# Kernel tuning notes

Measured on AMD Instinct MI355X. Metric: run time of the kernel, lower is better.

Reference implementation:

```python
import jax, jax.numpy as jnp
import numpy as np

N_NODES = 100000
N_EDGES = 1600000
D_IN = 128
D_HID = 128


def spmm(edge_row, edge_col, edge_val, x):
    # sparse [N,N] @ dense [N,D]: out[r] += val * x[c]
    gathered = edge_val[:, None] * x[edge_col]  # [E, D]
    return jax.ops.segment_sum(gathered, edge_row, num_segments=N_NODES)


def setup_inputs() -> dict:
    key = jax.random.key(0)
    ks = jax.random.split(key, 8)
    x = jax.random.normal(ks[0], (N_NODES, D_IN), dtype=jnp.float32)
    edge_row = jax.random.randint(ks[1], (N_EDGES,), 0, N_NODES, dtype=jnp.int32)
    edge_col = jax.random.randint(ks[2], (N_EDGES,), 0, N_NODES, dtype=jnp.int32)
    edge_val = jax.random.uniform(ks[3], (N_EDGES,), dtype=jnp.float32)
    s1 = 1.0 / np.sqrt(D_IN)
    s2 = 1.0 / np.sqrt(D_HID)
    W1 = jax.random.normal(ks[4], (D_IN, D_HID), dtype=jnp.float32) * s1
    b1 = jnp.zeros((D_HID,), dtype=jnp.float32)
    W2 = jax.random.normal(ks[5], (D_HID, D_HID), dtype=jnp.float32) * s2
    b2 = jnp.zeros((D_HID,), dtype=jnp.float32)
    Wout = jax.random.normal(ks[6], (D_HID, 1), dtype=jnp.float32) * s2
    bout = jnp.zeros((1,), dtype=jnp.float32)
    return {"x": x, "edge_row": edge_row, "edge_col": edge_col,
            "edge_val": edge_val, "W1": W1, "b1": b1, "W2": W2, "b2": b2,
            "Wout": Wout, "bout": bout}


def reference(x, edge_row, edge_col, edge_val, W1, b1, W2, b2, Wout, bout):
    # Layer 1: SpMM -> Linear -> ReLU (dropout = identity in eval)
    h = spmm(edge_row, edge_col, edge_val, x)
    h = jax.nn.relu(h @ W1 + b1)
    # Layer 2
    h = spmm(edge_row, edge_col, edge_val, h)
    h = jax.nn.relu(h @ W2 + b2)
    h = spmm(edge_row, edge_col, edge_val, h)
    out = h @ Wout + bout
    return jax.nn.softplus(out)
```

## Files before the change

### kernel.cpp

```cpp
#include <hip/hip_runtime.h>
#include <math.h>


typedef unsigned int u32;
typedef unsigned short u16;

__device__ inline float bf2f(u32 lo16){ return __uint_as_float(lo16 << 16); }
__device__ inline u32 f2bf(float f){
  u32 t = __float_as_uint(f);
  return (t + 0x7FFFu + ((t >> 16) & 1u)) >> 16;
}

__global__ void k_hist(const int* __restrict__ row, int* __restrict__ cnt, int E){
  int e = blockIdx.x*256 + threadIdx.x;
  if(e < E) atomicAdd(&cnt[__builtin_nontemporal_load(&row[e])], 1);
}

__global__ void k_scan1(const int* __restrict__ cnt, int* __restrict__ scanned,
                        int* __restrict__ sums, int n){
  __shared__ int tmp[1024];
  int i = blockIdx.x*1024 + threadIdx.x;
  int v = (i<n)? cnt[i] : 0;
  tmp[threadIdx.x] = v;
  __syncthreads();
  for(int off=1; off<1024; off<<=1){
    int t = (threadIdx.x>=off)? tmp[threadIdx.x-off] : 0;
    __syncthreads();
    tmp[threadIdx.x] += t;
    __syncthreads();
  }
  if(i<n) scanned[i] = tmp[threadIdx.x] - v;
  if(threadIdx.x==1023) sums[blockIdx.x] = tmp[1023];
}

__global__ void k_scan2(int* sums, int ntiles){
  if(threadIdx.x==0 && blockIdx.x==0){
    int acc=0;
    for(int i=0;i<ntiles;i++){ int v=sums[i]; sums[i]=acc; acc+=v; }
  }
}

__global__ void k_scan3(const int* __restrict__ scanned, const int* __restrict__ sums,
                        int* __restrict__ row_ptr, int* __restrict__ offs, int n, int E){
  int i = blockIdx.x*256 + threadIdx.x;
  if(i<n){ int ex = scanned[i] + sums[i>>10]; row_ptr[i]=ex; offs[i]=ex; }
  else if(i==n){ row_ptr[n]=E; }
}

__global__ __launch_bounds__(256) void k_scatter(const int* __restrict__ row,
                          const int* __restrict__ col,
                          const float* __restrict__ val, int* __restrict__ offs,
                          int2* __restrict__ pairs, int E, int N){
  const int r   = blockIdx.x & 7;
  const int sb  = blockIdx.x >> 3;
  const int nsb = gridDim.x >> 3;
  const int rpr = (N + 7) >> 3;
  const int lo  = r * rpr;
  const int hi  = min(lo + rpr, N);
  const int stride = nsb * 256;
  for(int e = sb*256 + threadIdx.x; e < E; e += stride){
    int rw = __builtin_nontemporal_load(&row[e]);
    if(rw >= lo && rw < hi){
      int   c = __builtin_nontemporal_load(&col[e]);
      float v = __builtin_nontemporal_load(&val[e]);
      int p = atomicAdd(&offs[rw], 1);
      pairs[p] = make_int2(c, __float_as_int(v));
    }
  }
}

template<bool A_BF16>
__global__ __launch_bounds__(256) void k_gemm(const void* __restrict__ Xv,
                                              const float* __restrict__ W,
                                              u16* __restrict__ Y, int n){
  __shared__ float xs_t[32][128];
  __shared__ float ws[32][128];
  const int t    = threadIdx.x;
  const int row0 = blockIdx.x * 128;
  const int cg   = t & 15;
  const int rg   = t >> 4;

  float acc[8][8];
  #pragma unroll
  for(int i=0;i<8;i++)
    #pragma unroll
    for(int j=0;j<8;j++) acc[i][j]=0.f;

  for(int kt=0; kt<128; kt+=32){
    {
      int r = t>>1, q = t&1;
      int gr = row0 + r;
      int kb = q*16;
      if(A_BF16){
        const u16* Xb = (const u16*)Xv;
        uint4 a = make_uint4(0,0,0,0), b = a;
        if(gr < n){
          const uint4* src = (const uint4*)(Xb + (size_t)gr*128 + kt + q*16);
          a = src[0]; b = src[1];
        }
        xs_t[kb+ 0][r]=bf2f(a.x&0xffff); xs_t[kb+ 1][r]=bf2f(a.x>>16);
        xs_t[kb+ 2][r]=bf2f(a.y&0xffff); xs_t[kb+ 3][r]=bf2f(a.y>>16);
        xs_t[kb+ 4][r]=bf2f(a.z&0xffff); xs_t[kb+ 5][r]=bf2f(a.z>>16);
        xs_t[kb+ 6][r]=bf2f(a.w&0xffff); xs_t[kb+ 7][r]=bf2f(a.w>>16);
        xs_t[kb+ 8][r]=bf2f(b.x&0xffff); xs_t[kb+ 9][r]=bf2f(b.x>>16);
        xs_t[kb+10][r]=bf2f(b.y&0xffff); xs_t[kb+11][r]=bf2f(b.y>>16);
        xs_t[kb+12][r]=bf2f(b.z&0xffff); xs_t[kb+13][r]=bf2f(b.z>>16);
        xs_t[kb+14][r]=bf2f(b.w&0xffff); xs_t[kb+15][r]=bf2f(b.w>>16);
      }else{
        const float* Xf = (const float*)Xv;
        float4 a = make_float4(0,0,0,0), b = a, c = a, d = a;
        if(gr < n){
          const float4* src = (const float4*)(Xf + (size_t)gr*128 + kt + q*16);
          a = src[0]; b = src[1]; c = src[2]; d = src[3];
        }
        xs_t[kb+ 0][r]=a.x; xs_t[kb+ 1][r]=a.y; xs_t[kb+ 2][r]=a.z; xs_t[kb+ 3][r]=a.w;
        xs_t[kb+ 4][r]=b.x; xs_t[kb+ 5][r]=b.y; xs_t[kb+ 6][r]=b.z; xs_t[kb+ 7][r]=b.w;
        xs_t[kb+ 8][r]=c.x; xs_t[kb+ 9][r]=c.y; xs_t[kb+10][r]=c.z; xs_t[kb+11][r]=c.w;
        xs_t[kb+12][r]=d.x; xs_t[kb+13][r]=d.y; xs_t[kb+14][r]=d.z; xs_t[kb+15][r]=d.w;
      }
    }
    #pragma unroll
    for(int rep=0; rep<4; rep++){
      int f  = t + rep*256;
      int kr = f >> 5;
      int cq = f & 31;
      float4 w = *(const float4*)(W + (size_t)(kt+kr)*128 + cq*4);
      *(float4*)&ws[kr][cq*4] = w;
    }
    __syncthreads();

    #pragma unroll
    for(int kk=0; kk<32; kk++){
      float4 wv0 = *(const float4*)&ws[kk][cg*8];
      float4 wv1 = *(const float4*)&ws[kk][cg*8+4];
      #pragma unroll
      for(int i=0;i<8;i++){
        float xv = xs_t[kk][rg*8+i];
        acc[i][0] = fmaf(xv, wv0.x, acc[i][0]);
        acc[i][1] = fmaf(xv, wv0.y, acc[i][1]);
        acc[i][2] = fmaf(xv, wv0.z, acc[i][2]);
        acc[i][3] = fmaf(xv, wv0.w, acc[i][3]);
        acc[i][4] = fmaf(xv, wv1.x, acc[i][4]);
        acc[i][5] = fmaf(xv, wv1.y, acc[i][5]);
        acc[i][6] = fmaf(xv, wv1.z, acc[i][6]);
        acc[i][7] = fmaf(xv, wv1.w, acc[i][7]);
      }
    }
    __syncthreads();
  }

  #pragma unroll
  for(int i=0;i<8;i++){
    int gr = row0 + rg*8 + i;
    if(gr < n){
      u32 w0 = f2bf(acc[i][0]) | (f2bf(acc[i][1])<<16);
      u32 w1 = f2bf(acc[i][2]) | (f2bf(acc[i][3])<<16);
      u32 w2 = f2bf(acc[i][4]) | (f2bf(acc[i][5])<<16);
      u32 w3 = f2bf(acc[i][6]) | (f2bf(acc[i][7])<<16);
      *(uint4*)(Y + (size_t)gr*128 + cg*8) = make_uint4(w0,w1,w2,w3);
    }
  }
}

__global__ __launch_bounds__(256) void k_spmm_relu(const int* __restrict__ row_ptr,
                                                   const int2* __restrict__ pairs,
                                                   const u16* __restrict__ y,
                                                   const float* __restrict__ bias,
                                                   u16* __restrict__ h, int n){
  int wid  = (int)((blockIdx.x*(size_t)blockDim.x + threadIdx.x) >> 6);
  int lane = threadIdx.x & 63;
  if(wid >= n) return;
  int s = row_ptr[wid], e = row_ptr[wid+1];
  float ax0=0.f, ay0=0.f, ax1=0.f, ay1=0.f, ax2=0.f, ay2=0.f, ax3=0.f, ay3=0.f;
  int i = s;
  for(; i+4 <= e; i += 4){
    int2 p0 = pairs[i], p1 = pairs[i+1], p2 = pairs[i+2], p3 = pairs[i+3];
    u32 w0 = ((const u32*)(y + (size_t)p0.x*128))[lane];
    u32 w1 = ((const u32*)(y + (size_t)p1.x*128))[lane];
    u32 w2 = ((const u32*)(y + (size_t)p2.x*128))[lane];
    u32 w3 = ((const u32*)(y + (size_t)p3.x*128))[lane];
    float v0 = __int_as_float(p0.y), v1 = __int_as_float(p1.y);
    float v2 = __int_as_float(p2.y), v3 = __int_as_float(p3.y);
    ax0 = fmaf(v0, bf2f(w0&0xffff), ax0); ay0 = fmaf(v0, bf2f(w0>>16), ay0);
    ax1 = fmaf(v1, bf2f(w1&0xffff), ax1); ay1 = fmaf(v1, bf2f(w1>>16), ay1);
    ax2 = fmaf(v2, bf2f(w2&0xffff), ax2); ay2 = fmaf(v2, bf2f(w2>>16), ay2);
    ax3 = fmaf(v3, bf2f(w3&0xffff), ax3); ay3 = fmaf(v3, bf2f(w3>>16), ay3);
  }
  for(; i < e; i++){
    int2 p = pairs[i];
    float v = __int_as_float(p.y);
    u32 w = ((const u32*)(y + (size_t)p.x*128))[lane];
    ax0 = fmaf(v, bf2f(w&0xffff), ax0); ay0 = fmaf(v, bf2f(w>>16), ay0);
  }
  float accx = (ax0+ax1)+(ax2+ax3);
  float accy = (ay0+ay1)+(ay2+ay3);
  float2 b = ((const float2*)bias)[lane];
  accx = fmaxf(accx + b.x, 0.f);
  accy = fmaxf(accy + b.y, 0.f);
  ((u32*)(h + (size_t)wid*128))[lane] = f2bf(accx) | (f2bf(accy)<<16);
}

__global__ __launch_bounds__(256) void k_spmm_head(const int* __restrict__ row_ptr,
                                                   const int2* __restrict__ pairs,
                                                   const u16* __restrict__ y,
                                                   const float* __restrict__ bias,
                                                   const float* __restrict__ Wout,
                                                   float* __restrict__ z, int n){
  int wid  = (int)((blockIdx.x*(size_t)blockDim.x + threadIdx.x) >> 6);
  int lane = threadIdx.x & 63;
  if(wid >= n) return;
  int s = row_ptr[wid], e = row_ptr[wid+1];
  float ax0=0.f, ay0=0.f, ax1=0.f, ay1=0.f, ax2=0.f, ay2=0.f, ax3=0.f, ay3=0.f;
  int i = s;
  for(; i+4 <= e; i += 4){
    int2 p0 = pairs[i], p1 = pairs[i+1], p2 = pairs[i+2], p3 = pairs[i+3];
    u32 w0 = ((const u32*)(y + (size_t)p0.x*128))[lane];
    u32 w1 = ((const u32*)(y + (size_t)p1.x*128))[lane];
    u32 w2 = ((const u32*)(y + (size_t)p2.x*128))[lane];
    u32 w3 = ((const u32*)(y + (size_t)p3.x*128))[lane];
    float v0 = __int_as_float(p0.y), v1 = __int_as_float(p1.y);
    float v2 = __int_as_float(p2.y), v3 = __int_as_float(p3.y);
    ax0 = fmaf(v0, bf2f(w0&0xffff), ax0); ay0 = fmaf(v0, bf2f(w0>>16), ay0);
    ax1 = fmaf(v1, bf2f(w1&0xffff), ax1); ay1 = fmaf(v1, bf2f(w1>>16), ay1);
    ax2 = fmaf(v2, bf2f(w2&0xffff), ax2); ay2 = fmaf(v2, bf2f(w2>>16), ay2);
    ax3 = fmaf(v3, bf2f(w3&0xffff), ax3); ay3 = fmaf(v3, bf2f(w3>>16), ay3);
  }
  for(; i < e; i++){
    int2 p = pairs[i];
    float v = __int_as_float(p.y);
    u32 w = ((const u32*)(y + (size_t)p.x*128))[lane];
    ax0 = fmaf(v, bf2f(w&0xffff), ax0); ay0 = fmaf(v, bf2f(w>>16), ay0);
  }
  float accx = (ax0+ax1)+(ax2+ax3);
  float accy = (ay0+ay1)+(ay2+ay3);
  float2 b  = ((const float2*)bias)[lane];
  float2 wv = ((const float2*)Wout)[lane];
  float hx = fmaxf(accx + b.x, 0.f);
  float hy = fmaxf(accy + b.y, 0.f);
  float p = hx*wv.x + hy*wv.y;
  #pragma unroll
  for(int off=32; off; off>>=1) p += __shfl_down(p, off);
  if(lane==0) z[wid] = p;
}

__global__ void k_spmm1_softplus(const int* __restrict__ row_ptr,
                                 const int2* __restrict__ pairs,
                                 const float* __restrict__ z,
                                 const float* __restrict__ bout,
                                 float* __restrict__ out, int n){
  int r = blockIdx.x*256 + threadIdx.x;
  if(r >= n) return;
  int s = row_ptr[r], e = row_ptr[r+1];
  float a0=0.f, a1=0.f, a2=0.f, a3=0.f;
  int i = s;
  for(; i+4 <= e; i += 4){
    int2 p0 = pairs[i],   p1 = pairs[i+1], p2 = pairs[i+2], p3 = pairs[i+3];
    a0 = fmaf(__int_as_float(p0.y), z[p0.x], a0);
    a1 = fmaf(__int_as_float(p1.y), z[p1.x], a1);
    a2 = fmaf(__int_as_float(p2.y), z[p2.x], a2);
    a3 = fmaf(__int_as_float(p3.y), z[p3.x], a3);
  }
  for(; i < e; i++){
    int2 p = pairs[i];
    a0 = fmaf(__int_as_float(p.y), z[p.x], a0);
  }
  float x = (a0+a1)+(a2+a3) + bout[0];
  out[r] = fmaxf(x, 0.f) + log1pf(expf(-fabsf(x)));
}

extern "C" void kernel_launch(void* const* d_in, const int* in_sizes, int n_in,
                              void* d_out, int out_size, void* d_ws, size_t ws_size,
                              hipStream_t stream){
  const float* x    = (const float*)d_in[0];
  const int*   erow = (const int*)d_in[1];
  const int*   ecol = (const int*)d_in[2];
  const float* eval = (const float*)d_in[3];
  const float* W1   = (const float*)d_in[4];
  const float* b1   = (const float*)d_in[5];
  const float* W2   = (const float*)d_in[6];
  const float* b2   = (const float*)d_in[7];
  const float* Wout = (const float*)d_in[8];
  const float* bout = (const float*)d_in[9];
  float* out = (float*)d_out;

  const int N = in_sizes[0] / 128;
  const int E = in_sizes[1];

  char* p = (char*)d_ws;
  auto alloc = [&](size_t bytes)->char*{
    char* r = p; p += (bytes + 255) & ~(size_t)255; return r;
  };
  int*   cnt     = (int*)  alloc((size_t)N*4);
  int*   row_ptr = (int*)  alloc((size_t)(N+1)*4);
  int*   offs    = (int*)  alloc((size_t)N*4);
  int*   scanned = (int*)  alloc((size_t)N*4);
  int*   sums    = (int*)  alloc(4096);
  int2*  pairs   = (int2*) alloc((size_t)E*8);
  u16*   ybuf    = (u16*)  alloc((size_t)N*128*2);
  u16*   hbuf    = (u16*)  alloc((size_t)N*128*2);
  float* z       = (float*)alloc((size_t)N*4);

  hipMemsetAsync(cnt, 0, (size_t)N*4, stream);
  k_hist<<<(E+255)/256, 256, 0, stream>>>(erow, cnt, E);
  int ntiles = (N+1023)/1024;
  k_scan1<<<ntiles, 1024, 0, stream>>>(cnt, scanned, sums, N);
  k_scan2<<<1, 64, 0, stream>>>(sums, ntiles);
  k_scan3<<<(N+1+255)/256, 256, 0, stream>>>(scanned, sums, row_ptr, offs, N, E);
  k_scatter<<<1024, 256, 0, stream>>>(erow, ecol, eval, offs, pairs, E, N);

  k_gemm<false><<<(N+127)/128, 256, 0, stream>>>(x, W1, ybuf, N);
  k_spmm_relu<<<(N+3)/4, 256, 0, stream>>>(row_ptr, pairs, ybuf, b1, hbuf, N);
  k_gemm<true><<<(N+127)/128, 256, 0, stream>>>(hbuf, W2, ybuf, N);
  k_spmm_head<<<(N+3)/4, 256, 0, stream>>>(row_ptr, pairs, ybuf, b2, Wout, z, N);
  k_spmm1_softplus<<<(N+255)/256, 256, 0, stream>>>(row_ptr, pairs, z, bout, out, N);
}
```

Measured before the change: 526.1 us.

## Replace FP32 FMA GEMM with bf16 MFMA GEMM using pre-transposed bf16 weights

The dense 128x128 GEMM now runs on bf16 MFMA instructions instead of scalar FP32 FMAs. The whole A tile and the weight matrix are staged in LDS with an XOR swizzle to avoid bank conflicts, and the weights are pre-converted and transposed by a small new kernel. Rounding the FP32 input x and the weights to bf16 adds precision loss, and the scalar per-element output stores are less coalesced than before. Nontemporal loads on row are also dropped in the hist and scatter kernels.

```diff
diff --git a/kernel.cpp b/kernel.cpp
--- a/kernel.cpp
+++ b/kernel.cpp
@@ -4,6 +4,8 @@
 
 typedef unsigned int u32;
 typedef unsigned short u16;
+typedef __attribute__((ext_vector_type(8))) short bf16x8;
+typedef __attribute__((ext_vector_type(4))) float f32x4;
 
 __device__ inline float bf2f(u32 lo16){ return __uint_as_float(lo16 << 16); }
 __device__ inline u32 f2bf(float f){
@@ -13,7 +15,7 @@
 
 __global__ void k_hist(const int* __restrict__ row, int* __restrict__ cnt, int E){
   int e = blockIdx.x*256 + threadIdx.x;
-  if(e < E) atomicAdd(&cnt[__builtin_nontemporal_load(&row[e])], 1);
+  if(e < E) atomicAdd(&cnt[row[e]], 1);
 }
 
 __global__ void k_scan1(const int* __restrict__ cnt, int* __restrict__ scanned,
@@ -59,7 +61,7 @@
   const int hi  = min(lo + rpr, N);
   const int stride = nsb * 256;
   for(int e = sb*256 + threadIdx.x; e < E; e += stride){
-    int rw = __builtin_nontemporal_load(&row[e]);
+    int rw = row[e];
     if(rw >= lo && rw < hi){
       int   c = __builtin_nontemporal_load(&col[e]);
       float v = __builtin_nontemporal_load(&val[e]);
@@ -69,95 +71,92 @@
   }
 }
 
+__global__ void k_cvtW(const float* __restrict__ W, u16* __restrict__ Wt){
+  int t = blockIdx.x*256 + threadIdx.x;
+  int nn = t >> 7, k = t & 127;
+  Wt[nn*128 + k] = (u16)f2bf(W[k*128 + nn]);
+}
+
 template<bool A_BF16>
 __global__ __launch_bounds__(256) void k_gemm(const void* __restrict__ Xv,
-                                              const float* __restrict__ W,
+                                              const u16* __restrict__ Wt,
                                               u16* __restrict__ Y, int n){
-  __shared__ float xs_t[32][128];
-  __shared__ float ws[32][128];
-  const int t    = threadIdx.x;
+  __shared__ u16 As[128*128];
+  __shared__ u16 Bs[128*128];
+  const int t = threadIdx.x;
   const int row0 = blockIdx.x * 128;
-  const int cg   = t & 15;
-  const int rg   = t >> 4;
-
-  float acc[8][8];
-  #pragma unroll
-  for(int i=0;i<8;i++)
+
+  {
+    int r = t>>1, q = t&1;
+    const uint4* src = (const uint4*)(Wt + r*128 + q*64);
     #pragma unroll
-    for(int j=0;j<8;j++) acc[i][j]=0.f;
-
-  for(int kt=0; kt<128; kt+=32){
-    {
-      int r = t>>1, q = t&1;
-      int gr = row0 + r;
-      int kb = q*16;
-      if(A_BF16){
-        const u16* Xb = (const u16*)Xv;
-        uint4 a = make_uint4(0,0,0,0), b = a;
-        if(gr < n){
-          const uint4* src = (const uint4*)(Xb + (size_t)gr*128 + kt + q*16);
-          a = src[0]; b = src[1];
-        }
-        xs_t[kb+ 0][r]=bf2f(a.x&0xffff); xs_t[kb+ 1][r]=bf2f(a.x>>16);
-        xs_t[kb+ 2][r]=bf2f(a.y&0xffff); xs_t[kb+ 3][r]=bf2f(a.y>>16);
-        xs_t[kb+ 4][r]=bf2f(a.z&0xffff); xs_t[kb+ 5][r]=bf2f(a.z>>16);
-        xs_t[kb+ 6][r]=bf2f(a.w&0xffff); xs_t[kb+ 7][r]=bf2f(a.w>>16);
-        xs_t[kb+ 8][r]=bf2f(b.x&0xffff); xs_t[kb+ 9][r]=bf2f(b.x>>16);
-        xs_t[kb+10][r]=bf2f(b.y&0xffff); xs_t[kb+11][r]=bf2f(b.y>>16);
-        xs_t[kb+12][r]=bf2f(b.z&0xffff); xs_t[kb+13][r]=bf2f(b.z>>16);
-        xs_t[kb+14][r]=bf2f(b.w&0xffff); xs_t[kb+15][r]=bf2f(b.w>>16);
-      }else{
-        const float* Xf = (const float*)Xv;
-        float4 a = make_float4(0,0,0,0), b = a, c = a, d = a;
-        if(gr < n){
-          const float4* src = (const float4*)(Xf + (size_t)gr*128 + kt + q*16);
-          a = src[0]; b = src[1]; c = src[2]; d = src[3];
-        }
-        xs_t[kb+ 0][r]=a.x; xs_t[kb+ 1][r]=a.y; xs_t[kb+ 2][r]=a.z; xs_t[kb+ 3][r]=a.w;
-        xs_t[kb+ 4][r]=b.x; xs_t[kb+ 5][r]=b.y; xs_t[kb+ 6][r]=b.z; xs_t[kb+ 7][r]=b.w;
-        xs_t[kb+ 8][r]=c.x; xs_t[kb+ 9][r]=c.y; xs_t[kb+10][r]=c.z; xs_t[kb+11][r]=c.w;
-        xs_t[kb+12][r]=d.x; xs_t[kb+13][r]=d.y; xs_t[kb+14][r]=d.z; xs_t[kb+15][r]=d.w;
-      }
-    }
-    #pragma unroll
-    for(int rep=0; rep<4; rep++){
-      int f  = t + rep*256;
-      int kr = f >> 5;
-      int cq = f & 31;
-      float4 w = *(const float4*)(W + (size_t)(kt+kr)*128 + cq*4);
-      *(float4*)&ws[kr][cq*4] = w;
-    }
-    __syncthreads();
-
-    #pragma unroll
-    for(int kk=0; kk<32; kk++){
-      float4 wv0 = *(const float4*)&ws[kk][cg*8];
-      float4 wv1 = *(const float4*)&ws[kk][cg*8+4];
+    for(int i=0;i<8;i++){
+      uint4 v = src[i];
+      int c = q*8 + i;
+      *(uint4*)&Bs[r*128 + ((c ^ (r&15))<<3)] = v;
+    }
+  }
+  {
+    int r = t>>1, q = t&1;
+    int gr = row0 + r;
+    if(A_BF16){
+      const uint4* src = (const uint4*)((const u16*)Xv + (size_t)gr*128 + q*64);
+      uint4 z = make_uint4(0,0,0,0);
       #pragma unroll
       for(int i=0;i<8;i++){
-        float xv = xs_t[kk][rg*8+i];
-        acc[i][0] = fmaf(xv, wv0.x, acc[i][0]);
-        acc[i][1] = fmaf(xv, wv0.y, acc[i][1]);
-        acc[i][2] = fmaf(xv, wv0.z, acc[i][2]);
-        acc[i][3] = fmaf(xv, wv0.w, acc[i][3]);
-        acc[i][4] = fmaf(xv, wv1.x, acc[i][4]);
-        acc[i][5] = fmaf(xv, wv1.y, acc[i][5]);
-        acc[i][6] = fmaf(xv, wv1.z, acc[i][6]);
-        acc[i][7] = fmaf(xv, wv1.w, acc[i][7]);
+        uint4 v = (gr<n)? src[i] : z;
+        int c = q*8 + i;
+        *(uint4*)&As[r*128 + ((c ^ (r&15))<<3)] = v;
       }
-    }
-    __syncthreads();
-  }
-
+    }else{
+      const float4* src = (const float4*)((const float*)Xv + (size_t)gr*128 + q*64);
+      float4 z4 = make_float4(0,0,0,0);
+      #pragma unroll
+      for(int i=0;i<8;i++){
+        float4 a = (gr<n)? src[2*i]   : z4;
+        float4 b = (gr<n)? src[2*i+1] : z4;
+        uint4 v = make_uint4(f2bf(a.x)|(f2bf(a.y)<<16), f2bf(a.z)|(f2bf(a.w)<<16),
+                             f2bf(b.x)|(f2bf(b.y)<<16), f2bf(b.z)|(f2bf(b.w)<<16));
+        int c = q*8 + i;
+        *(uint4*)&As[r*128 + ((c ^ (r&15))<<3)] = v;
+      }
+    }
+  }
+  __syncthreads();
+
+  const int w  = t>>6, l = t&63;
+  const int lr = l & 15;
+  const int kg = l >> 4;
+  f32x4 acc[2][8];
   #pragma unroll
-  for(int i=0;i<8;i++){
-    int gr = row0 + rg*8 + i;
-    if(gr < n){
-      u32 w0 = f2bf(acc[i][0]) | (f2bf(acc[i][1])<<16);
-      u32 w1 = f2bf(acc[i][2]) | (f2bf(acc[i][3])<<16);
-      u32 w2 = f2bf(acc[i][4]) | (f2bf(acc[i][5])<<16);
-      u32 w3 = f2bf(acc[i][6]) | (f2bf(acc[i][7])<<16);
-      *(uint4*)(Y + (size_t)gr*128 + cg*8) = make_uint4(w0,w1,w2,w3);
+  for(int mi=0;mi<2;mi++)
+    #pragma unroll
+    for(int ni=0;ni<8;ni++) acc[mi][ni] = (f32x4){0.f,0.f,0.f,0.f};
+
+  #pragma unroll
+  for(int kt=0; kt<4; kt++){
+    int c = kt*4 + kg;
+    bf16x8 a0 = *(const bf16x8*)&As[(w*32 + lr)*128      + ((c ^ lr)<<3)];
+    bf16x8 a1 = *(const bf16x8*)&As[(w*32 + 16 + lr)*128 + ((c ^ lr)<<3)];
+    #pragma unroll
+    for(int ni=0; ni<8; ni++){
+      bf16x8 b = *(const bf16x8*)&Bs[(ni*16 + lr)*128 + ((c ^ lr)<<3)];
+      acc[0][ni] = __builtin_amdgcn_mfma_f32_16x16x32_bf16(a0, b, acc[0][ni], 0,0,0);
+      acc[1][ni] = __builtin_amdgcn_mfma_f32_16x16x32_bf16(a1, b, acc[1][ni], 0,0,0);
+    }
+  }
+
+  #pragma unroll
+  for(int mi=0;mi<2;mi++){
+    #pragma unroll
+    for(int r=0;r<4;r++){
+      int grow = row0 + w*32 + mi*16 + kg*4 + r;
+      if(grow < n){
+        #pragma unroll
+        for(int ni=0;ni<8;ni++){
+          Y[(size_t)grow*128 + ni*16 + lr] = (u16)f2bf(acc[mi][ni][r]);
+        }
+      }
     }
   }
 }
@@ -299,6 +298,8 @@
   u16*   ybuf    = (u16*)  alloc((size_t)N*128*2);
   u16*   hbuf    = (u16*)  alloc((size_t)N*128*2);
   float* z       = (float*)alloc((size_t)N*4);
+  u16*   Wt1     = (u16*)  alloc(128*128*2);
+  u16*   Wt2     = (u16*)  alloc(128*128*2);
 
   hipMemsetAsync(cnt, 0, (size_t)N*4, stream);
   k_hist<<<(E+255)/256, 256, 0, stream>>>(erow, cnt, E);
@@ -308,9 +309,12 @@
   k_scan3<<<(N+1+255)/256, 256, 0, stream>>>(scanned, sums, row_ptr, offs, N, E);
   k_scatter<<<1024, 256, 0, stream>>>(erow, ecol, eval, offs, pairs, E, N);
 
-  k_gemm<false><<<(N+127)/128, 256, 0, stream>>>(x, W1, ybuf, N);
+  k_cvtW<<<64, 256, 0, stream>>>(W1, Wt1);
+  k_cvtW<<<64, 256, 0, stream>>>(W2, Wt2);
+
+  k_gemm<false><<<(N+127)/128, 256, 0, stream>>>(x, Wt1, ybuf, N);
   k_spmm_relu<<<(N+3)/4, 256, 0, stream>>>(row_ptr, pairs, ybuf, b1, hbuf, N);
-  k_gemm<true><<<(N+127)/128, 256, 0, stream>>>(hbuf, W2, ybuf, N);
+  k_gemm<true><<<(N+127)/128, 256, 0, stream>>>(hbuf, Wt2, ybuf, N);
   k_spmm_head<<<(N+3)/4, 256, 0, stream>>>(row_ptr, pairs, ybuf, b2, Wout, z, N);
   k_spmm1_softplus<<<(N+255)/256, 256, 0, stream>>>(row_ptr, pairs, z, bout, out, N);
 }
```

Result: faster. 499.4 us (-5.1%).
